# Optimization experiments

Hardware: AMD Instinct MI355X
Metric: run time of the kernel (lower is better)

## Reference

```python
import jax, jax.numpy as jnp
from jax import lax
import numpy as np

NUM_FILTERS = 24
NUM_BASIS = 31
GAMMA = 0.5


def setup_inputs() -> dict:
    key = jax.random.key(0)
    k1, k2, k3, k4 = jax.random.split(key, 4)
    B, H, W = 8, 512, 512
    u = jax.random.uniform(k1, (B, 1, H, W), dtype=jnp.float32)
    f = jax.random.uniform(k2, (B, 1, H, W), dtype=jnp.float32)
    filters = jax.random.normal(k3, (NUM_FILTERS, 1, 5, 5), dtype=jnp.float32) * 0.08
    # each RBFInfluence: mu = linspace(-1,1,31) (identical init per filter), weights = randn*0.1
    mu = jnp.tile(jnp.linspace(-1.0, 1.0, NUM_BASIS, dtype=jnp.float32)[None, :], (NUM_FILTERS, 1))
    weights = jax.random.normal(k4, (NUM_FILTERS, NUM_BASIS), dtype=jnp.float32) * 0.1
    lambda_param = jnp.float32(0.15)
    return {"u": u, "f": f, "filters": filters, "mu": mu, "weights": weights,
            "lambda_param": lambda_param}


def _avg_pool3(x):
    # F.avg_pool2d(kernel=3, stride=1, padding=1), count_include_pad=True -> always /9
    s = lax.reduce_window(x, 0.0, lax.add, (1, 1, 3, 3), (1, 1, 1, 1),
                          [(0, 0), (0, 0), (1, 1), (1, 1)])
    return s / 9.0


def reference(u, f, filters, mu, weights, lambda_param):
    u = jnp.clip(u, 1e-4, 1.0)
    f = jnp.clip(f, 1e-4, 1.0)
    dn = ("NCHW", "OIHW", "NCHW")
    # all per-filter 5x5 convs batched as one conv: [B,1,H,W] -> [B,K,H,W]
    conv = lax.conv_general_dilated(u, filters, (1, 1), [(2, 2), (2, 2)], dimension_numbers=dn)
    # RBF influence per filter: phi = sum_j w[c,j] * exp(-(conv - mu[c,j])^2 / (2*gamma^2))
    inv2g2 = 1.0 / (2.0 * GAMMA * GAMMA)
    phi = jnp.zeros_like(conv)
    for j in range(NUM_BASIS):  # small fixed loop; avoids [B,K,H,W,31] intermediate
        d = conv - mu[:, j][None, :, None, None]
        phi = phi + weights[:, j][None, :, None, None] * jnp.exp(-(d * d) * inv2g2)
    # u_sigma / M identical across filter loop iterations in the original -> hoisted
    u_sigma = _avg_pool3(u)  # [B,1,H,W]
    M = jnp.mean(u_sigma) + 0.001
    scaled_phi = (u_sigma / M) * phi  # [B,K,H,W]
    # sum_i conv2d(scaled_phi_i, flip(k_i)) == single conv with [1,K,5,5] kernel
    kT = jnp.transpose(jnp.flip(filters, axis=(2, 3)), (1, 0, 2, 3))  # [1,K,5,5]
    diffusion = lax.conv_general_dilated(scaled_phi, kT, (1, 1), [(2, 2), (2, 2)],
                                         dimension_numbers=dn)  # [B,1,H,W]
    reaction = lambda_param * (u - f) / (u + 0.05)
    return jnp.clip(u - diffusion - reaction, 0.0, 1.0)
```

## Files before the change

### kernel.cpp

```cpp
#include <hip/hip_runtime.h>
#include <hip/hip_fp16.h>
#include <math.h>

#define NBATCH 8
#define HH 512
#define WW 512
#define NF 24
#define NB 31
#define TH 32
#define TW 64
#define STRIP 16
#define UH 40
#define UW 72
#define SU_S 76
#define UGH 36
#define UG_S 76
#define SPH 20
#define SP_S 72
#define NTHR 128
#define LUTN 256
#define WS_LO 8
#define WS_SC 40
#define WS_LUT 72
#define WS_PART (WS_LUT + NF * LUTN)
#define WS_REQ ((WS_PART + 1024) * 4)

__device__ __forceinline__ void wave_lds_fence() {
    asm volatile("s_waitcnt lgkmcnt(0)" ::: "memory");
    __builtin_amdgcn_wave_barrier();
}

__device__ __forceinline__ int sp_col(int r, int c) {
    return (c < 64) ? (c ^ (((r >> 2) & 3) << 3)) : c;
}

__device__ __forceinline__ void phi_pair(const float* mu, const float* wts, int c,
                                         float x, float h, float* p0, float* p1) {
    float a = 0.f, b = 0.f;
    for (int j = 0; j < NB; ++j) {
        float m = mu[c * NB + j], w = wts[c * NB + j];
        float d0 = x - m, d1 = x + h - m;
        a += w * __expf(-2.f * d0 * d0);
        b += w * __expf(-2.f * d1 * d1);
    }
    *p0 = a; *p1 = b;
}

__device__ __forceinline__ void filter_range(const float* filt, int c,
                                             float* lo_, float* rng_) {
    float lo = 0.f, hi = 0.f;
    for (int i = 0; i < 25; ++i) {
        float k = filt[c * 25 + i];
        lo += fminf(k, 0.f);
        hi += fmaxf(k, 0.f);
    }
    *lo_ = lo;
    *rng_ = fmaxf(hi - lo, 1e-9f);
}

__global__ __launch_bounds__(256) void pre_kernel(const float* __restrict__ u,
                                                  const float* __restrict__ filt,
                                                  const float* __restrict__ mu,
                                                  const float* __restrict__ wts,
                                                  float* __restrict__ ws, int do_lut) {
    __shared__ float sred[4];
    const int tid = threadIdx.x;
    const int N = NBATCH * HH * WW;
    int stride = gridDim.x * blockDim.x;
    float s = 0.f;
    for (int i = blockIdx.x * blockDim.x + tid; i < N; i += stride) {
        int x = i & (WW - 1);
        int y = (i >> 9) & (HH - 1);
        float v = fminf(fmaxf(u[i], 1e-4f), 1.0f);
        float wy = (y == 0 || y == HH - 1) ? 2.f : 3.f;
        float wx = (x == 0 || x == WW - 1) ? 2.f : 3.f;
        s += v * (wy * wx);
    }
#pragma unroll
    for (int off = 32; off > 0; off >>= 1) s += __shfl_down(s, off, 64);
    if ((tid & 63) == 0) sred[tid >> 6] = s;
    __syncthreads();
    if (tid == 0) ws[WS_PART + blockIdx.x] = sred[0] + sred[1] + sred[2] + sred[3];

    if (do_lut && blockIdx.x < NF) {
        const int c = blockIdx.x;
        float lo, rng;
        filter_range(filt, c, &lo, &rng);
        float h = rng * (1.f / 255.f);
        float p0, p1;
        phi_pair(mu, wts, c, lo + (float)tid * h, h, &p0, &p1);
        unsigned u0 = (unsigned)__half_as_ushort(__float2half(p0));
        unsigned u1 = (unsigned)__half_as_ushort(__float2half(p1));
        ((unsigned*)ws)[WS_LUT + c * LUTN + tid] = u0 | (u1 << 16);
        if (tid == 0) { ws[WS_LO + c] = lo; ws[WS_SC + c] = 255.f / rng; }
    }
}

template <bool WSLUT>
__global__ __launch_bounds__(NTHR, 2) void tnrd_kernel(
    const float* __restrict__ u, const float* __restrict__ f,
    const float* __restrict__ filt, const float* __restrict__ mu,
    const float* __restrict__ wts, const float* __restrict__ lamp,
    const float* __restrict__ ws, float* __restrict__ out)
{
    __shared__ float su[UH][SU_S];
    __shared__ float ug[UGH][UG_S];
    __shared__ float spb[2][SPH][SP_S];
    __shared__ unsigned slut[2][2][LUTN];
    __shared__ float sred[2];

    const int tid = threadIdx.x;
    const int w = tid >> 6;
    const int lane = tid & 63;
    const int bz = blockIdx.z;
    const int oy0 = blockIdx.y * TH;
    const int ox0 = blockIdx.x * TW;
    const float* ub = u + bz * HH * WW;
    const unsigned* lutg = (const unsigned*)ws + WS_LUT;

    for (int i = tid; i < UH * UW; i += NTHR) {
        int uy = i / UW, ux = i - uy * UW;
        int gy = oy0 - 4 + uy, gx = ox0 - 4 + ux;
        float v = 0.f;
        if ((unsigned)gy < (unsigned)HH && (unsigned)gx < (unsigned)WW)
            v = fminf(fmaxf(ub[gy * WW + gx], 1e-4f), 1.0f);
        su[uy][ux] = v;
    }

    {
        float ps = 0.f;
#pragma unroll
        for (int j = 0; j < 1024 / NTHR; ++j) ps += ws[WS_PART + j * NTHR + tid];
#pragma unroll
        for (int off = 32; off > 0; off >>= 1) ps += __shfl_down(ps, off, 64);
        if (lane == 0) sred[w] = ps;
    }

    if (WSLUT) {
        ((uint4*)&slut[w][0][0])[lane] = ((const uint4*)lutg)[lane];
    }
    __syncthreads();

    const float tot = sred[0] + sred[1];
    const float Mv = tot * (1.0f / (9.0f * NBATCH * HH * WW)) + 0.001f;
    const float inv9M = (1.f / 9.f) / Mv;

    for (int i = tid; i < UGH * 17; i += NTHR) {
        int r = i / 17, t = i - r * 17;
        int c0 = 4 * t;
        float s4[4] = {0.f, 0.f, 0.f, 0.f};
#pragma unroll
        for (int dy = 0; dy < 3; ++dy) {
            float4 a = *(const float4*)&su[r + 1 + dy][c0];
            float4 b = *(const float4*)&su[r + 1 + dy][c0 + 4];
            float t8[8] = {a.x, a.y, a.z, a.w, b.x, b.y, b.z, b.w};
#pragma unroll
            for (int k = 0; k < 4; ++k) s4[k] += t8[k + 1] + t8[k + 2] + t8[k + 3];
        }
        int gy = oy0 - 2 + r;
        bool ry = (unsigned)gy < (unsigned)HH;
        float o[4];
#pragma unroll
        for (int k = 0; k < 4; ++k) {
            int gx = ox0 - 2 + c0 + k;
            o[k] = (ry && (unsigned)gx < (unsigned)WW) ? s4[k] * inv9M : 0.f;
        }
        *(float4*)&ug[r][c0] = make_float4(o[0], o[1], o[2], o[3]);
    }
    __syncthreads();

    float dif[4][4] = {{0.f}};
    const int or0 = 4 * (lane >> 4);
    const int oc0 = 4 * (lane & 15);
    const int wy = w * STRIP;
    float (*spw)[SP_S] = spb[w];

    for (int c = 0; c < NF; ++c) {
        const float* fc = filt + c * 25;
        float lo, scc;
        uint4 nlut;
        const bool havepre = WSLUT && (c + 1 < NF);
        if (havepre) nlut = ((const uint4*)(lutg + (c + 1) * LUTN))[lane];
        if (WSLUT) {
            lo = ws[WS_LO + c]; scc = ws[WS_SC + c];
        } else {
            float rng; filter_range(filt, c, &lo, &rng); scc = 255.f / rng;
            float h = rng * (1.f / 255.f);
            for (int e = lane; e < LUTN; e += 64) {
                float p0, p1;
                phi_pair(mu, wts, c, lo + (float)e * h, h, &p0, &p1);
                unsigned u0 = (unsigned)__half_as_ushort(__float2half(p0));
                unsigned u1 = (unsigned)__half_as_ushort(__float2half(p1));
                slut[w][c & 1][e] = u0 | (u1 << 16);
            }
        }
        const float offc = -lo * scc;
        const unsigned* sl = &slut[w][c & 1][0];
        wave_lds_fence();

#pragma unroll
        for (int p = 0; p < 3; ++p) {
            int task = p * 64 + lane;
            if (task < 170) {
                int tr = task / 17, tc2 = task - tr * 17;
                int sr0 = 2 * tr, sc0 = 4 * tc2;
                float acc[2][4] = {{0.f}};
#pragma unroll
                for (int ky = 0; ky < 6; ++ky) {
                    float4 a = *(const float4*)&su[wy + sr0 + ky][sc0];
                    float4 b = *(const float4*)&su[wy + sr0 + ky][sc0 + 4];
                    float t8[8] = {a.x, a.y, a.z, a.w, b.x, b.y, b.z, b.w};
#pragma unroll
                    for (int r = 0; r < 2; ++r) {
                        int kyy = ky - r;
                        if (kyy < 0 || kyy > 4) continue;
#pragma unroll
                        for (int dx = 0; dx < 5; ++dx) {
                            float wgt = fc[kyy * 5 + dx];
#pragma unroll
                            for (int k = 0; k < 4; ++k)
                                acc[r][k] = fmaf(wgt, t8[k + dx], acc[r][k]);
                        }
                    }
                }
#pragma unroll
                for (int r = 0; r < 2; ++r) {
                    float4 uu = *(const float4*)&ug[wy + sr0 + r][sc0];
                    float uu4[4] = {uu.x, uu.y, uu.z, uu.w};
                    float o[4];
#pragma unroll
                    for (int k = 0; k < 4; ++k) {
                        float t = fmaf(acc[r][k], scc, offc);
                        t = fminf(fmaxf(t, 0.f), 254.999f);
                        int i0 = (int)t;
                        float fr = t - (float)i0;
                        unsigned pk = sl[i0];
                        __half2 hv = *reinterpret_cast<const __half2*>(&pk);
                        float2 fv = __half22float2(hv);
                        o[k] = fmaf(fr, fv.y - fv.x, fv.x) * uu4[k];
                    }
                    *(float4*)&spw[sr0 + r][sp_col(sr0 + r, sc0)] =
                        make_float4(o[0], o[1], o[2], o[3]);
                }
            }
        }
        wave_lds_fence();

#pragma unroll
        for (int s = 0; s < 8; ++s) {
            int rr = or0 + s;
            float4 a = *(const float4*)&spw[rr][sp_col(rr, oc0)];
            float4 b = *(const float4*)&spw[rr][sp_col(rr, oc0 + 4)];
            float t8[8] = {a.x, a.y, a.z, a.w, b.x, b.y, b.z, b.w};
#pragma unroll
            for (int r = 0; r < 4; ++r) {
                int dy = s - r;
                if (dy < 0 || dy > 4) continue;
#pragma unroll
                for (int dx = 0; dx < 5; ++dx) {
                    float wgt = fc[(4 - dy) * 5 + (4 - dx)];
#pragma unroll
                    for (int k = 0; k < 4; ++k)
                        dif[r][k] = fmaf(wgt, t8[k + dx], dif[r][k]);
                }
            }
        }

        if (havepre) ((uint4*)&slut[w][(c + 1) & 1][0])[lane] = nlut;
    }

    {
        const float lam = lamp[0];
        const float* fb = f + bz * HH * WW;
        float* ob = out + bz * HH * WW;
#pragma unroll
        for (int r = 0; r < 4; ++r) {
            int gy = oy0 + wy + or0 + r;
            int gx = ox0 + oc0;
            float4 uv4 = *(const float4*)&su[wy + or0 + r + 4][oc0 + 4];
            float4 fv4 = *(const float4*)&fb[gy * WW + gx];
            float uu[4] = {uv4.x, uv4.y, uv4.z, uv4.w};
            float ff[4] = {fv4.x, fv4.y, fv4.z, fv4.w};
            float o[4];
#pragma unroll
            for (int k = 0; k < 4; ++k) {
                float uv = uu[k];
                float fv = fminf(fmaxf(ff[k], 1e-4f), 1.0f);
                float reac = lam * (uv - fv) / (uv + 0.05f);
                o[k] = fminf(fmaxf(uv - dif[r][k] - reac, 0.f), 1.f);
            }
            *(float4*)&ob[gy * WW + gx] = make_float4(o[0], o[1], o[2], o[3]);
        }
    }
}

extern "C" void kernel_launch(void* const* d_in, const int* in_sizes, int n_in,
                              void* d_out, int out_size, void* d_ws, size_t ws_size,
                              hipStream_t stream) {
    const float* u = (const float*)d_in[0];
    const float* f = (const float*)d_in[1];
    const float* filt = (const float*)d_in[2];
    const float* mu = (const float*)d_in[3];
    const float* wts = (const float*)d_in[4];
    const float* lam = (const float*)d_in[5];
    float* ws = (float*)d_ws;
    float* out = (float*)d_out;

    const bool use_ws = ws_size >= (size_t)WS_REQ;
    pre_kernel<<<1024, 256, 0, stream>>>(u, filt, mu, wts, ws, use_ws ? 1 : 0);
    dim3 grid(WW / TW, HH / TH, NBATCH);
    if (use_ws)
        tnrd_kernel<true><<<grid, NTHR, 0, stream>>>(u, f, filt, mu, wts, lam, ws, out);
    else
        tnrd_kernel<false><<<grid, NTHR, 0, stream>>>(u, f, filt, mu, wts, lam, ws, out);
}
```

Before: 211.1 us.

## Enlarge tile to 64x64 with 512 threads, fp16 scaled-phi and software-pipelined filter stages

Changes the block from two independent 16-row wave strips to a 64x64 tile shared by 512 threads. The scaled-phi intermediate for filter c+1 is computed into a double buffer while the second convolution for filter c reads the other buffer, with block barriers between stages. The intermediate is stored as packed fp16, and the 3x3 average pool reuses horizontal sums across row pairs. The larger tile is meant to cut halo recomputation and LDS footprint, at the cost of block-wide syncs and extra fp16 rounding error.

```diff
diff --git a/kernel.cpp b/kernel.cpp
--- a/kernel.cpp
+++ b/kernel.cpp
@@ -7,32 +7,23 @@
 #define WW 512
 #define NF 24
 #define NB 31
-#define TH 32
+#define TH 64
 #define TW 64
-#define STRIP 16
-#define UH 40
+#define UH 72
 #define UW 72
 #define SU_S 76
-#define UGH 36
-#define UG_S 76
-#define SPH 20
-#define SP_S 72
-#define NTHR 128
+#define UGH 68
+#define UG_S 72
+#define SPH 68
+#define SP_WS 36
+#define NTHR 512
+#define SP_TASKS 578
 #define LUTN 256
 #define WS_LO 8
 #define WS_SC 40
 #define WS_LUT 72
 #define WS_PART (WS_LUT + NF * LUTN)
 #define WS_REQ ((WS_PART + 1024) * 4)
-
-__device__ __forceinline__ void wave_lds_fence() {
-    asm volatile("s_waitcnt lgkmcnt(0)" ::: "memory");
-    __builtin_amdgcn_wave_barrier();
-}
-
-__device__ __forceinline__ int sp_col(int r, int c) {
-    return (c < 64) ? (c ^ (((r >> 2) & 3) << 3)) : c;
-}
 
 __device__ __forceinline__ void phi_pair(const float* mu, const float* wts, int c,
                                          float x, float h, float* p0, float* p1) {
@@ -97,7 +88,7 @@
 }
 
 template <bool WSLUT>
-__global__ __launch_bounds__(NTHR, 2) void tnrd_kernel(
+__global__ __launch_bounds__(NTHR, 4) void tnrd_kernel(
     const float* __restrict__ u, const float* __restrict__ f,
     const float* __restrict__ filt, const float* __restrict__ mu,
     const float* __restrict__ wts, const float* __restrict__ lamp,
@@ -105,13 +96,11 @@
 {
     __shared__ float su[UH][SU_S];
     __shared__ float ug[UGH][UG_S];
-    __shared__ float spb[2][SPH][SP_S];
-    __shared__ unsigned slut[2][2][LUTN];
-    __shared__ float sred[2];
+    __shared__ unsigned spw[2][SPH][SP_WS];
+    __shared__ unsigned slut[2][LUTN];
+    __shared__ float sred[8];
 
     const int tid = threadIdx.x;
-    const int w = tid >> 6;
-    const int lane = tid & 63;
     const int bz = blockIdx.z;
     const int oy0 = blockIdx.y * TH;
     const int ox0 = blockIdx.x * TW;
@@ -127,146 +116,184 @@
         su[uy][ux] = v;
     }
 
+    if (WSLUT) {
+        if (tid < 2 * LUTN) {
+            int cc = tid >> 8, e = tid & 255;
+            slut[cc][e] = lutg[cc * LUTN + e];
+        }
+    } else {
+        for (int cc = 0; cc < 2; ++cc) {
+            if (tid < LUTN) {
+                float lo, rng;
+                filter_range(filt, cc, &lo, &rng);
+                float h = rng * (1.f / 255.f);
+                float p0, p1;
+                phi_pair(mu, wts, cc, lo + (float)tid * h, h, &p0, &p1);
+                unsigned u0 = (unsigned)__half_as_ushort(__float2half(p0));
+                unsigned u1 = (unsigned)__half_as_ushort(__float2half(p1));
+                slut[cc][tid] = u0 | (u1 << 16);
+            }
+        }
+    }
+
     {
-        float ps = 0.f;
-#pragma unroll
-        for (int j = 0; j < 1024 / NTHR; ++j) ps += ws[WS_PART + j * NTHR + tid];
+        float ps = ws[WS_PART + tid] + ws[WS_PART + NTHR + tid];
 #pragma unroll
         for (int off = 32; off > 0; off >>= 1) ps += __shfl_down(ps, off, 64);
-        if (lane == 0) sred[w] = ps;
-    }
-
-    if (WSLUT) {
-        ((uint4*)&slut[w][0][0])[lane] = ((const uint4*)lutg)[lane];
+        if ((tid & 63) == 0) sred[tid >> 6] = ps;
     }
     __syncthreads();
 
-    const float tot = sred[0] + sred[1];
+    float tot = 0.f;
+#pragma unroll
+    for (int j = 0; j < 8; ++j) tot += sred[j];
     const float Mv = tot * (1.0f / (9.0f * NBATCH * HH * WW)) + 0.001f;
     const float inv9M = (1.f / 9.f) / Mv;
 
-    for (int i = tid; i < UGH * 17; i += NTHR) {
-        int r = i / 17, t = i - r * 17;
-        int c0 = 4 * t;
-        float s4[4] = {0.f, 0.f, 0.f, 0.f};
-#pragma unroll
-        for (int dy = 0; dy < 3; ++dy) {
-            float4 a = *(const float4*)&su[r + 1 + dy][c0];
-            float4 b = *(const float4*)&su[r + 1 + dy][c0 + 4];
+    for (int t = tid; t < SP_TASKS; t += NTHR) {
+        int tr = t / 17, tc = t - tr * 17;
+        int y0 = 2 * tr, x0 = 4 * tc;
+        float hr[4][4];
+#pragma unroll
+        for (int j = 0; j < 4; ++j) {
+            float4 a = *(const float4*)&su[y0 + 1 + j][x0];
+            float4 b = *(const float4*)&su[y0 + 1 + j][x0 + 4];
             float t8[8] = {a.x, a.y, a.z, a.w, b.x, b.y, b.z, b.w};
 #pragma unroll
-            for (int k = 0; k < 4; ++k) s4[k] += t8[k + 1] + t8[k + 2] + t8[k + 3];
-        }
-        int gy = oy0 - 2 + r;
-        bool ry = (unsigned)gy < (unsigned)HH;
-        float o[4];
-#pragma unroll
-        for (int k = 0; k < 4; ++k) {
-            int gx = ox0 - 2 + c0 + k;
-            o[k] = (ry && (unsigned)gx < (unsigned)WW) ? s4[k] * inv9M : 0.f;
-        }
-        *(float4*)&ug[r][c0] = make_float4(o[0], o[1], o[2], o[3]);
+            for (int k = 0; k < 4; ++k) hr[j][k] = t8[k + 1] + t8[k + 2] + t8[k + 3];
+        }
+#pragma unroll
+        for (int r = 0; r < 2; ++r) {
+            int gy = oy0 - 2 + y0 + r;
+            bool ry = (unsigned)gy < (unsigned)HH;
+            float o[4];
+#pragma unroll
+            for (int k = 0; k < 4; ++k) {
+                int gx = ox0 - 2 + x0 + k;
+                o[k] = (ry && (unsigned)gx < (unsigned)WW)
+                         ? (hr[r][k] + hr[r + 1][k] + hr[r + 2][k]) * inv9M : 0.f;
+            }
+            *(float4*)&ug[y0 + r][x0] = make_float4(o[0], o[1], o[2], o[3]);
+        }
     }
     __syncthreads();
 
-    float dif[4][4] = {{0.f}};
-    const int or0 = 4 * (lane >> 4);
-    const int oc0 = 4 * (lane & 15);
-    const int wy = w * STRIP;
-    float (*spw)[SP_S] = spb[w];
-
-    for (int c = 0; c < NF; ++c) {
+    auto sp_phase = [&](int c, int buf) {
         const float* fc = filt + c * 25;
         float lo, scc;
-        uint4 nlut;
-        const bool havepre = WSLUT && (c + 1 < NF);
-        if (havepre) nlut = ((const uint4*)(lutg + (c + 1) * LUTN))[lane];
-        if (WSLUT) {
-            lo = ws[WS_LO + c]; scc = ws[WS_SC + c];
-        } else {
-            float rng; filter_range(filt, c, &lo, &rng); scc = 255.f / rng;
-            float h = rng * (1.f / 255.f);
-            for (int e = lane; e < LUTN; e += 64) {
-                float p0, p1;
-                phi_pair(mu, wts, c, lo + (float)e * h, h, &p0, &p1);
-                unsigned u0 = (unsigned)__half_as_ushort(__float2half(p0));
-                unsigned u1 = (unsigned)__half_as_ushort(__float2half(p1));
-                slut[w][c & 1][e] = u0 | (u1 << 16);
-            }
-        }
+        if (WSLUT) { lo = ws[WS_LO + c]; scc = ws[WS_SC + c]; }
+        else { float rng; filter_range(filt, c, &lo, &rng); scc = 255.f / rng; }
         const float offc = -lo * scc;
-        const unsigned* sl = &slut[w][c & 1][0];
-        wave_lds_fence();
-
-#pragma unroll
-        for (int p = 0; p < 3; ++p) {
-            int task = p * 64 + lane;
-            if (task < 170) {
-                int tr = task / 17, tc2 = task - tr * 17;
-                int sr0 = 2 * tr, sc0 = 4 * tc2;
-                float acc[2][4] = {{0.f}};
-#pragma unroll
-                for (int ky = 0; ky < 6; ++ky) {
-                    float4 a = *(const float4*)&su[wy + sr0 + ky][sc0];
-                    float4 b = *(const float4*)&su[wy + sr0 + ky][sc0 + 4];
-                    float t8[8] = {a.x, a.y, a.z, a.w, b.x, b.y, b.z, b.w};
-#pragma unroll
-                    for (int r = 0; r < 2; ++r) {
-                        int kyy = ky - r;
-                        if (kyy < 0 || kyy > 4) continue;
-#pragma unroll
-                        for (int dx = 0; dx < 5; ++dx) {
-                            float wgt = fc[kyy * 5 + dx];
-#pragma unroll
-                            for (int k = 0; k < 4; ++k)
-                                acc[r][k] = fmaf(wgt, t8[k + dx], acc[r][k]);
-                        }
+        const unsigned* sl = &slut[buf][0];
+        for (int t = tid; t < SP_TASKS; t += NTHR) {
+            int tr = t / 17, tc = t - tr * 17;
+            int y0 = 2 * tr, x0 = 4 * tc;
+            float acc[2][4] = {{0.f}};
+#pragma unroll
+            for (int ky = 0; ky < 6; ++ky) {
+                float4 a = *(const float4*)&su[y0 + ky][x0];
+                float4 b = *(const float4*)&su[y0 + ky][x0 + 4];
+                float t8[8] = {a.x, a.y, a.z, a.w, b.x, b.y, b.z, b.w};
+#pragma unroll
+                for (int r = 0; r < 2; ++r) {
+                    int kyy = ky - r;
+                    if (kyy < 0 || kyy > 4) continue;
+#pragma unroll
+                    for (int dx = 0; dx < 5; ++dx) {
+                        float wgt = fc[kyy * 5 + dx];
+#pragma unroll
+                        for (int k = 0; k < 4; ++k)
+                            acc[r][k] = fmaf(wgt, t8[k + dx], acc[r][k]);
                     }
                 }
-#pragma unroll
-                for (int r = 0; r < 2; ++r) {
-                    float4 uu = *(const float4*)&ug[wy + sr0 + r][sc0];
-                    float uu4[4] = {uu.x, uu.y, uu.z, uu.w};
-                    float o[4];
-#pragma unroll
-                    for (int k = 0; k < 4; ++k) {
-                        float t = fmaf(acc[r][k], scc, offc);
-                        t = fminf(fmaxf(t, 0.f), 254.999f);
-                        int i0 = (int)t;
-                        float fr = t - (float)i0;
+            }
+#pragma unroll
+            for (int r = 0; r < 2; ++r) {
+                float4 uu = *(const float4*)&ug[y0 + r][x0];
+                float uu4[4] = {uu.x, uu.y, uu.z, uu.w};
+                unsigned pw[2];
+#pragma unroll
+                for (int half = 0; half < 2; ++half) {
+                    float o0, o1;
+#pragma unroll
+                    for (int k2 = 0; k2 < 2; ++k2) {
+                        int k = half * 2 + k2;
+                        float t2 = fmaf(acc[r][k], scc, offc);
+                        t2 = fminf(fmaxf(t2, 0.f), 254.999f);
+                        int i0 = (int)t2;
+                        float fr = t2 - (float)i0;
                         unsigned pk = sl[i0];
                         __half2 hv = *reinterpret_cast<const __half2*>(&pk);
                         float2 fv = __half22float2(hv);
-                        o[k] = fmaf(fr, fv.y - fv.x, fv.x) * uu4[k];
+                        float v = fmaf(fr, fv.y - fv.x, fv.x) * uu4[k];
+                        if (k2 == 0) o0 = v; else o1 = v;
                     }
-                    *(float4*)&spw[sr0 + r][sp_col(sr0 + r, sc0)] =
-                        make_float4(o[0], o[1], o[2], o[3]);
+                    unsigned w0 = (unsigned)__half_as_ushort(__float2half(o0));
+                    unsigned w1 = (unsigned)__half_as_ushort(__float2half(o1));
+                    pw[half] = w0 | (w1 << 16);
                 }
-            }
-        }
-        wave_lds_fence();
-
-#pragma unroll
-        for (int s = 0; s < 8; ++s) {
-            int rr = or0 + s;
-            float4 a = *(const float4*)&spw[rr][sp_col(rr, oc0)];
-            float4 b = *(const float4*)&spw[rr][sp_col(rr, oc0 + 4)];
-            float t8[8] = {a.x, a.y, a.z, a.w, b.x, b.y, b.z, b.w};
-#pragma unroll
-            for (int r = 0; r < 4; ++r) {
-                int dy = s - r;
-                if (dy < 0 || dy > 4) continue;
-#pragma unroll
-                for (int dx = 0; dx < 5; ++dx) {
-                    float wgt = fc[(4 - dy) * 5 + (4 - dx)];
-#pragma unroll
-                    for (int k = 0; k < 4; ++k)
-                        dif[r][k] = fmaf(wgt, t8[k + dx], dif[r][k]);
+                *(uint2*)&spw[buf][y0 + r][x0 >> 1] = make_uint2(pw[0], pw[1]);
+            }
+        }
+    };
+
+    float dif[2][4] = {{0.f}};
+    const int tr2 = tid >> 4;
+    const int tc2 = tid & 15;
+    const int or0 = 2 * tr2, oc0 = 4 * tc2;
+    const int wrd0 = oc0 >> 1;
+
+    sp_phase(0, 0);
+    __syncthreads();
+
+    for (int c = 0; c < NF; ++c) {
+        unsigned nl = 0;
+        const bool hp = WSLUT && (c + 2 < NF) && (tid < LUTN);
+        if (hp) nl = lutg[(c + 2) * LUTN + tid];
+
+        if (c + 1 < NF) sp_phase(c + 1, (c + 1) & 1);
+
+        {
+            const float* fc = filt + c * 25;
+            const unsigned (*spc)[SP_WS] = spw[c & 1];
+#pragma unroll
+            for (int s = 0; s < 6; ++s) {
+                uint2 a = *(const uint2*)&spc[or0 + s][wrd0];
+                uint2 b = *(const uint2*)&spc[or0 + s][wrd0 + 2];
+                float2 f0 = __half22float2(*reinterpret_cast<const __half2*>(&a.x));
+                float2 f1 = __half22float2(*reinterpret_cast<const __half2*>(&a.y));
+                float2 f2 = __half22float2(*reinterpret_cast<const __half2*>(&b.x));
+                float2 f3 = __half22float2(*reinterpret_cast<const __half2*>(&b.y));
+                float t8[8] = {f0.x, f0.y, f1.x, f1.y, f2.x, f2.y, f3.x, f3.y};
+#pragma unroll
+                for (int r = 0; r < 2; ++r) {
+                    int dy = s - r;
+                    if (dy < 0 || dy > 4) continue;
+#pragma unroll
+                    for (int dx = 0; dx < 5; ++dx) {
+                        float wgt = fc[(4 - dy) * 5 + (4 - dx)];
+#pragma unroll
+                        for (int k = 0; k < 4; ++k)
+                            dif[r][k] = fmaf(wgt, t8[k + dx], dif[r][k]);
+                    }
                 }
             }
         }
 
-        if (havepre) ((uint4*)&slut[w][(c + 1) & 1][0])[lane] = nlut;
+        if (!WSLUT && (c + 2 < NF) && tid < LUTN) {
+            int cn = c + 2;
+            float lo, rng;
+            filter_range(filt, cn, &lo, &rng);
+            float h = rng * (1.f / 255.f);
+            float p0, p1;
+            phi_pair(mu, wts, cn, lo + (float)tid * h, h, &p0, &p1);
+            unsigned u0 = (unsigned)__half_as_ushort(__float2half(p0));
+            unsigned u1 = (unsigned)__half_as_ushort(__float2half(p1));
+            slut[c & 1][tid] = u0 | (u1 << 16);
+        }
+        if (hp) slut[c & 1][tid] = nl;
+
+        if (c < NF - 1) __syncthreads();
     }
 
     {
@@ -274,10 +301,10 @@
         const float* fb = f + bz * HH * WW;
         float* ob = out + bz * HH * WW;
 #pragma unroll
-        for (int r = 0; r < 4; ++r) {
-            int gy = oy0 + wy + or0 + r;
+        for (int r = 0; r < 2; ++r) {
+            int gy = oy0 + or0 + r;
             int gx = ox0 + oc0;
-            float4 uv4 = *(const float4*)&su[wy + or0 + r + 4][oc0 + 4];
+            float4 uv4 = *(const float4*)&su[or0 + r + 4][oc0 + 4];
             float4 fv4 = *(const float4*)&fb[gy * WW + gx];
             float uu[4] = {uv4.x, uv4.y, uv4.z, uv4.w};
             float ff[4] = {fv4.x, fv4.y, fv4.z, fv4.w};
```

Result: faster. 203.4 us (-3.6%).
